# Performance work log

Measured on AMD Instinct MI355X. Metric: run time of the kernel, lower is better.

The kernel has to match this reference:

```python
import jax, jax.numpy as jnp
import numpy as np

EPS_NORM = 1e-12
BN_EPS = 1e-5

def _l2norm(x, axis=-1):
    n = jnp.sqrt(jnp.sum(x * x, axis=axis, keepdims=True))
    return x / jnp.maximum(n, EPS_NORM)

def setup_inputs() -> dict:
    key = jax.random.key(0)
    ks = jax.random.split(key, 16)
    B, C, H, W, K = 32, 256, 64, 64, 5
    supp_feat = jax.random.normal(ks[0], (B, C, H, W), dtype=jnp.float32)
    supp_mask = (jax.random.uniform(ks[1], (B, 1, H, W)) > 0.5).astype(jnp.float32)
    part_queries = 0.02 * jax.random.normal(ks[2], (1, K, C), dtype=jnp.float32)
    temperature = jnp.array([0.1], dtype=jnp.float32)
    margin = jnp.array([0.15], dtype=jnp.float32)
    q_w = jax.random.normal(ks[3], (C, C), dtype=jnp.float32) / np.sqrt(C)  # 1x1 conv, no bias
    bn_w = 1.0 + 0.1 * jax.random.normal(ks[4], (C,), dtype=jnp.float32)
    bn_b = 0.1 * jax.random.normal(ks[5], (C,), dtype=jnp.float32)
    bn_mean = 0.1 * jax.random.normal(ks[6], (C,), dtype=jnp.float32)
    bn_var = 0.5 + jax.random.uniform(ks[7], (C,), dtype=jnp.float32)
    k_w = jax.random.normal(ks[8], (C, C), dtype=jnp.float32) / np.sqrt(C)
    k_b = 0.01 * jax.random.normal(ks[9], (C,), dtype=jnp.float32)
    v_w = jax.random.normal(ks[10], (C, C), dtype=jnp.float32) / np.sqrt(C)
    v_b = 0.01 * jax.random.normal(ks[11], (C,), dtype=jnp.float32)
    out_w = jax.random.normal(ks[12], (C, C), dtype=jnp.float32) / np.sqrt(C)
    out_b = 0.01 * jax.random.normal(ks[13], (C,), dtype=jnp.float32)
    gamma = jnp.array([0.1], dtype=jnp.float32)  # nonzero so the refine branch contributes
    return {"supp_feat": supp_feat, "supp_mask": supp_mask, "part_queries": part_queries,
            "temperature": temperature, "margin": margin, "q_w": q_w, "bn_w": bn_w,
            "bn_b": bn_b, "bn_mean": bn_mean, "bn_var": bn_var, "k_w": k_w, "k_b": k_b,
            "v_w": v_w, "v_b": v_b, "out_w": out_w, "out_b": out_b, "gamma": gamma}

def reference(supp_feat, supp_mask, part_queries, temperature, margin, q_w, bn_w, bn_b,
              bn_mean, bn_var, k_w, k_b, v_w, v_b, out_w, out_b, gamma):
    B, C, H, W = supp_feat.shape
    K = part_queries.shape[1]
    flat_mask = supp_mask.reshape(B, -1)                       # [B, HW]
    flat_feat = jnp.swapaxes(supp_feat.reshape(B, C, -1), 1, 2)  # [B, HW, C]
    queries_norm = _l2norm(part_queries)[0]                    # [K, C]
    feat_norm = _l2norm(flat_feat)                             # [B, HW, C]
    temp = jnp.maximum(temperature, 0.01)[0]
    sim = jnp.einsum('kc,bnc->bkn', queries_norm, feat_norm) / temp  # [B, K, HW]
    sim = jnp.where(flat_mask[:, None, :] > 0, sim, -jnp.inf)
    attn = jnp.nan_to_num(jax.nn.softmax(sim, axis=-1), nan=0.0)
    part_tokens = jnp.einsum('bkn,bnc->bkc', attn, flat_feat)  # [B, K, C]
    # diversity loss
    nt = _l2norm(part_tokens)
    cos = jnp.einsum('bkc,bjc->bkj', nt, nt) * (1.0 - jnp.eye(K, dtype=supp_feat.dtype))
    m = jnp.clip(margin, 0.0, 0.5)[0]
    div_loss = jnp.maximum(cos - m, 0.0).sum() / (B * K * (K - 1) + 1e-5)
    # refine attention
    q = jnp.einsum('oc,bchw->bohw', q_w, supp_feat)            # 1x1 conv, no bias
    scale = bn_w / jnp.sqrt(bn_var + BN_EPS)
    q = q * scale[None, :, None, None] + (bn_b - bn_mean * scale)[None, :, None, None]
    Q = jnp.swapaxes(q.reshape(B, C, -1), 1, 2)                # [B, HW, C]
    Kt = part_tokens @ k_w.T + k_b                             # [B, K, C]
    Vt = part_tokens @ v_w.T + v_b
    refine = jax.nn.softmax(jnp.einsum('bnc,bkc->bnk', Q, Kt) / (C ** 0.5), axis=-1)
    attn_out = jnp.einsum('bnk,bkc->bnc', refine, Vt)          # [B, HW, C]
    attn_out = jnp.swapaxes(attn_out, 1, 2).reshape(B, C, H, W)
    attn_out = jnp.einsum('oc,bchw->bohw', out_w, attn_out) + out_b[None, :, None, None]
    enhanced = supp_feat + gamma[0] * attn_out
    return (enhanced, div_loss, part_tokens)
```

## Files before the change

### kernel.cpp

```cpp
#include <hip/hip_runtime.h>
#include <hip/hip_bf16.h>
#include <math.h>

#define B_  32
#define C_  256
#define HW_ 4096
#define K_  5
#define P_  128
#define NT_ 32
#define PS_ 68

typedef __hip_bfloat16 bf16;
typedef unsigned int u32;
typedef __attribute__((ext_vector_type(8))) short bf16x8;
typedef __attribute__((ext_vector_type(4))) float f32x4;

template<bool BF>
__device__ inline float LD(const void* p, size_t i) {
    if (BF) return __bfloat162float(((const bf16*)p)[i]);
    return ((const float*)p)[i];
}
template<bool BF>
__device__ inline void ST(void* p, size_t i, float v) {
    if (BF) ((bf16*)p)[i] = __float2bfloat16(v);
    else    ((float*)p)[i] = v;
}
template<bool BF>
__device__ inline float4 LD4(const void* p, size_t i) {
    if (BF) {
        ushort4 u = *(const ushort4*)((const unsigned short*)p + i);
        float4 r;
        r.x = __uint_as_float(((u32)u.x) << 16);
        r.y = __uint_as_float(((u32)u.y) << 16);
        r.z = __uint_as_float(((u32)u.z) << 16);
        r.w = __uint_as_float(((u32)u.w) << 16);
        return r;
    }
    return *(const float4*)((const float*)p + i);
}
template<bool BF>
__device__ inline void ST2(void* p, size_t i, float2 v) {
    if (BF) {
        bf16 a = __float2bfloat16(v.x), b = __float2bfloat16(v.y);
        ushort2 u;
        u.x = *(unsigned short*)&a; u.y = *(unsigned short*)&b;
        *(ushort2*)((unsigned short*)p + i) = u;
    } else {
        *(float2*)((float*)p + i) = v;
    }
}
__device__ inline u32 packbf2(float a, float b) {
    bf16 x = __float2bfloat16(a), y = __float2bfloat16(b);
    return (((u32)*(unsigned short*)&y) << 16) | (u32)(*(unsigned short*)&x);
}
__device__ inline float lo16f(u32 u) { return __uint_as_float(u << 16); }
__device__ inline float hi16f(u32 u) { return __uint_as_float(u & 0xffff0000u); }

__device__ int detect_bf(const void* feat, int* cntL) {
    int t = threadIdx.x;
    if (t == 0) *cntL = 0;
    __syncthreads();
    const unsigned short* u = (const unsigned short*)feat;
    int local = 0;
    for (int i = t; i < 4096; i += blockDim.x) {
        float v = __uint_as_float(((u32)u[i]) << 16);
        float a = fabsf(v);
        local += (a >= 1e-4f && a <= 100.f) ? 1 : 0;
    }
    for (int o = 32; o > 0; o >>= 1) local += __shfl_down(local, o, 64);
    if ((t & 63) == 0) atomicAdd(cntL, local);
    __syncthreads();
    return (*cntL > 3072) ? 1 : 0;
}

__device__ inline float blk_sum(float v, float* sh) {
    for (int o = 32; o > 0; o >>= 1) v += __shfl_down(v, o, 64);
    int w = threadIdx.x >> 6;
    __syncthreads();
    if ((threadIdx.x & 63) == 0) sh[w] = v;
    __syncthreads();
    return sh[0] + sh[1] + sh[2] + sh[3];
}

template<bool BF>
__device__ void simpt_body(const void* feat, const void* mask, const void* temp,
                           const void* pq, float* ptp, float* mz, float* smem) {
    u32*   featB = (u32*)smem;
    float* red   = smem + 17408;
    u32*   wB    = (u32*)red;
    float* qL    = smem + 17408 + 1536;
    float* simL  = qL;
    float* sc    = qL + 1280;
    int t = threadIdx.x, lane = t & 63, q = t >> 6;
    int b = blockIdx.y, tile = blockIdx.x;

    if (q < K_) {
        float4 v = LD4<BF>(pq, (size_t)q * C_ + lane * 4);
        float ss = v.x * v.x + v.y * v.y + v.z * v.z + v.w * v.w;
        for (int o = 32; o > 0; o >>= 1) ss += __shfl_xor(ss, o, 64);
        float inv = 1.0f / fmaxf(sqrtf(ss), 1e-12f);
        *(float4*)(qL + q * C_ + lane * 4) =
            make_float4(v.x * inv, v.y * inv, v.z * inv, v.w * inv);
    }
    if (t == 0) sc[0] = 1.0f / fmaxf(LD<BF>(temp, 0), 0.01f);
    __syncthreads();

    int c0 = q * 32, half = lane >> 5, lm = lane & 31;
    float sa[4] = {0.f, 0.f, 0.f, 0.f};
    float da[K_][4];
    #pragma unroll
    for (int k = 0; k < K_; k++)
        #pragma unroll
        for (int i = 0; i < 4; i++) da[k][i] = 0.f;
    size_t gbase = (size_t)b * C_ * HW_ + (size_t)tile * P_ + lm * 4;
    #pragma unroll 4
    for (int j = 0; j < 16; j++) {
        int c = c0 + 2 * j + half;
        float4 f = LD4<BF>(feat, gbase + (size_t)c * HW_);
        sa[0] += f.x * f.x; sa[1] += f.y * f.y; sa[2] += f.z * f.z; sa[3] += f.w * f.w;
        #pragma unroll
        for (int k = 0; k < K_; k++) {
            float qv = qL[k * C_ + c];
            da[k][0] += f.x * qv; da[k][1] += f.y * qv;
            da[k][2] += f.z * qv; da[k][3] += f.w * qv;
        }
        *(uint2*)&featB[c * PS_ + 2 * lm] =
            make_uint2(packbf2(f.x, f.y), packbf2(f.z, f.w));
    }
    #pragma unroll
    for (int i = 0; i < 4; i++) sa[i] += __shfl_down(sa[i], 32, 64);
    #pragma unroll
    for (int k = 0; k < K_; k++)
        #pragma unroll
        for (int i = 0; i < 4; i++) da[k][i] += __shfl_down(da[k][i], 32, 64);

    float tinv = sc[0];
    for (int r = 0; r < 4; r++) {
        if (lane < 32) {
            red[0 * 256 + q * 32 + lane] = sa[r];
            #pragma unroll
            for (int k = 0; k < K_; k++) red[(1 + k) * 256 + q * 32 + lane] = da[k][r];
        }
        __syncthreads();
        if (t < 160) {
            int kk = t >> 5, m = t & 31, n = 4 * m + r;
            float ssum = 0.f, dsum = 0.f;
            #pragma unroll
            for (int g = 0; g < 8; g++) {
                ssum += red[0 * 256 + g * 32 + m];
                dsum += red[(1 + kk) * 256 + g * 32 + m];
            }
            float mval = LD<BF>(mask, (size_t)b * HW_ + tile * P_ + n);
            simL[kk * P_ + n] = (mval > 0.f)
                ? dsum * (tinv / fmaxf(sqrtf(ssum), 1e-12f)) : -INFINITY;
        }
        __syncthreads();
    }

    if (q < K_) {
        float s0 = simL[q * P_ + 2 * lane], s1 = simL[q * P_ + 2 * lane + 1];
        float m = fmaxf(s0, s1);
        for (int o = 32; o > 0; o >>= 1) m = fmaxf(m, __shfl_xor(m, o, 64));
        float e0 = (s0 == -INFINITY) ? 0.f : __expf(s0 - m);
        float e1 = (s1 == -INFINITY) ? 0.f : __expf(s1 - m);
        float z = e0 + e1;
        for (int o = 32; o > 0; o >>= 1) z += __shfl_xor(z, o, 64);
        wB[q * PS_ + lane] = packbf2(e0, e1);
        if (lane == 0) {
            size_t mzb = ((size_t)(b * NT_ + tile) * K_ + q) * 2;
            mz[mzb] = m; mz[mzb + 1] = z;
        }
    }
    __syncthreads();

    int r16 = lane & 15, g = lane >> 4;
    size_t pb = (size_t)(b * NT_ + tile) * (K_ * C_);
    #pragma unroll
    for (int sub = 0; sub < 2; sub++) {
        int ctile = q * 32 + sub * 16;
        f32x4 acc = {0.f, 0.f, 0.f, 0.f};
        #pragma unroll
        for (int s = 0; s < 4; s++) {
            bf16x8 a = *(const bf16x8*)(featB + (ctile + r16) * PS_ + 16 * s + 4 * g);
            bf16x8 bb = *(const bf16x8*)(wB + r16 * PS_ + 16 * s + 4 * g);
            acc = __builtin_amdgcn_mfma_f32_16x16x32_bf16(a, bb, acc, 0, 0, 0);
        }
        if (r16 < K_) {
            #pragma unroll
            for (int r = 0; r < 4; r++)
                ptp[pb + (size_t)r16 * C_ + ctile + 4 * g + r] = acc[r];
        }
    }
}
__global__ __launch_bounds__(512, 4) void k_simpt(const void* feat, const void* mask,
                                                  const void* temp, const void* pq,
                                                  float* ptp, float* mz) {
    __shared__ __attribute__((aligned(16))) float smem[20232];
    __shared__ int cnt;
    int flg = detect_bf(feat, &cnt);
    if (flg) simpt_body<true >(feat, mask, temp, pq, ptp, mz, smem);
    else     simpt_body<false>(feat, mask, temp, pq, ptp, mz, smem);
}

__device__ inline float merge_one(const float* ptp, const float* mz,
                                  int b, int kk, int c) {
    float M = -INFINITY;
    #pragma unroll 8
    for (int tl = 0; tl < NT_; tl++)
        M = fmaxf(M, mz[((size_t)(b * NT_ + tl) * K_ + kk) * 2]);
    float Zs = 0.f, acc = 0.f;
    #pragma unroll 8
    for (int tl = 0; tl < NT_; tl++) {
        size_t mzb = ((size_t)(b * NT_ + tl) * K_ + kk) * 2;
        float m_t = mz[mzb], z_t = mz[mzb + 1];
        float s = (m_t == -INFINITY) ? 0.f : __expf(m_t - M);
        Zs += z_t * s;
        acc += ptp[(size_t)(b * NT_ + tl) * (K_ * C_) + kk * C_ + c] * s;
    }
    return (Zs > 0.f) ? acc / Zs : 0.f;
}
template<bool BF>
__device__ void prep_part(const void* qw, const void* kw, const void* kb,
                          const void* vw, const void* vb, const void* ow,
                          const void* bnw, const void* bnb, const void* bnm,
                          const void* bnv, float ptv, int bk,
                          float* W2, float* b2, float* OV, float* pt, float* smem) {
    float* ptL = smem;
    float* KtL = smem + 256;
    float* VtL = smem + 512;
    float* sh  = smem + 768;
    int t = threadIdx.x;
    ptL[t] = ptv;
    pt[(size_t)bk * C_ + t] = ptv;
    __syncthreads();
    float kt = LD<BF>(kb, t), vt = LD<BF>(vb, t);
    for (int c = 0; c < C_; c += 4) {
        float4 p4 = *(float4*)(ptL + c);
        float4 kw4 = LD4<BF>(kw, (size_t)t * C_ + c);
        float4 vw4 = LD4<BF>(vw, (size_t)t * C_ + c);
        kt += kw4.x * p4.x + kw4.y * p4.y + kw4.z * p4.z + kw4.w * p4.w;
        vt += vw4.x * p4.x + vw4.y * p4.y + vw4.z * p4.z + vw4.w * p4.w;
    }
    float scale = LD<BF>(bnw, t) * rsqrtf(LD<BF>(bnv, t) + 1e-5f);
    float shift = LD<BF>(bnb, t) - LD<BF>(bnm, t) * scale;
    KtL[t] = kt * scale;
    VtL[t] = vt;
    float bpart = kt * shift;
    __syncthreads();
    float ov = 0;
    for (int c = 0; c < C_; c += 4) {
        float4 v4 = *(float4*)(VtL + c);
        float4 ow4 = LD4<BF>(ow, (size_t)t * C_ + c);
        ov += ow4.x * v4.x + ow4.y * v4.y + ow4.z * v4.z + ow4.w * v4.w;
    }
    OV[(size_t)bk * C_ + t] = ov;
    float w2 = 0;
    for (int o = 0; o < C_; o++) w2 += KtL[o] * LD<BF>(qw, (size_t)o * C_ + t);
    W2[(size_t)bk * C_ + t] = w2 * (1.0f / 16.0f);
    float bs = blk_sum(bpart, sh);
    if (t == 0) b2[bk] = bs * (1.0f / 16.0f);
}
template<bool BF>
__device__ void div_part(const float* ptp, const float* mz, const void* margin,
                         float* divpart, float* smem) {
    float* ptL = smem;
    float* rn  = smem + K_ * C_;
    float* sh  = rn + 8;
    int b = blockIdx.x - B_ * K_, t = threadIdx.x;
    for (int kk = 0; kk < K_; kk++) ptL[kk * C_ + t] = merge_one(ptp, mz, b, kk, t);
    __syncthreads();
    for (int k = 0; k < K_; k++) {
        float v = ptL[k * C_ + t];
        float s = blk_sum(v * v, sh);
        if (t == 0) rn[k] = 1.0f / fmaxf(sqrtf(s), 1e-12f);
    }
    __syncthreads();
    float m = LD<BF>(margin, 0);
    m = fminf(fmaxf(m, 0.f), 0.5f);
    int p = t >> 3, g = t & 7;
    float contrib = 0.f;
    if (p < K_ * K_) {
        int k = p / K_, j = p % K_;
        float d = 0;
        for (int c = g; c < C_; c += 8) d += ptL[k * C_ + c] * ptL[j * C_ + c];
        d += __shfl_down(d, 4, 8);
        d += __shfl_down(d, 2, 8);
        d += __shfl_down(d, 1, 8);
        if (g == 0 && k != j) contrib = fmaxf(d * rn[k] * rn[j] - m, 0.f);
    }
    float s = blk_sum(contrib, sh);
    if (t == 0) divpart[b] = s;
}
template<bool BF>
__device__ void mergeprep_body(const void* qw, const void* kw, const void* kb,
                               const void* vw, const void* vb, const void* ow,
                               const void* bnw, const void* bnb, const void* bnm,
                               const void* bnv, const void* margin,
                               const float* ptp, const float* mz,
                               float* W2, float* b2, float* OV, float* pt,
                               float* divpart, float* smem) {
    int bid = blockIdx.x, t = threadIdx.x;
    if (bid < B_ * K_) {
        int b = bid / K_, kk = bid % K_;
        float ptv = merge_one(ptp, mz, b, kk, t);
        prep_part<BF>(qw, kw, kb, vw, vb, ow, bnw, bnb, bnm, bnv,
                      ptv, bid, W2, b2, OV, pt, smem);
    } else {
        div_part<BF>(ptp, mz, margin, divpart, smem);
    }
}
__global__ void k_mergeprep(const void* feat, const void* qw, const void* kw,
                            const void* kb, const void* vw, const void* vb,
                            const void* ow, const void* bnw, const void* bnb,
                            const void* bnm, const void* bnv, const void* margin,
                            const float* ptp, const float* mz,
                            float* W2, float* b2, float* OV, float* pt, float* divpart) {
    __shared__ __attribute__((aligned(16))) float smem[K_ * C_ + 16];
    __shared__ int cnt;
    int flg = detect_bf(feat, &cnt);
    if (flg) mergeprep_body<true >(qw, kw, kb, vw, vb, ow, bnw, bnb, bnm, bnv, margin,
                                   ptp, mz, W2, b2, OV, pt, divpart, smem);
    else     mergeprep_body<false>(qw, kw, kb, vw, vb, ow, bnw, bnb, bnm, bnv, margin,
                                   ptp, mz, W2, b2, OV, pt, divpart, smem);
}

template<bool BF>
__device__ void fin_body(const void* feat, const void* outb, const void* gamma,
                         const float* W2, const float* b2, const float* OV,
                         const float* pt, const float* divpart,
                         void* dout, float* smem) {
    u32*   featU = (u32*)smem;
    float* red   = smem + 16384;
    float* eL    = red + 1280;
    u32*   W2p   = (u32*)(eL + 640);
    u32*   OVp   = W2p + 640;
    float* obL   = (float*)(OVp + 640);
    float* b2L   = obL + 256;
    int t = threadIdx.x, lane = t & 63, q = t >> 6;
    int b = blockIdx.y, tile = blockIdx.x;
    for (int i = t; i < 640; i += 512) {
        W2p[i] = packbf2(W2[(size_t)b * 1280 + 2 * i], W2[(size_t)b * 1280 + 2 * i + 1]);
        OVp[i] = packbf2(OV[(size_t)b * 1280 + 2 * i], OV[(size_t)b * 1280 + 2 * i + 1]);
    }
    if (t < C_) obL[t] = LD<BF>(outb, t);
    if (t < K_) b2L[t] = b2[b * K_ + t];
    __syncthreads();

    int c0 = q * 32, half = lane >> 5, lm = lane & 31;
    size_t gbase = (size_t)b * C_ * HW_ + (size_t)tile * P_ + lm * 4;
    float la[K_][4];
    #pragma unroll
    for (int k = 0; k < K_; k++)
        #pragma unroll
        for (int i = 0; i < 4; i++) la[k][i] = 0.f;
    #pragma unroll 4
    for (int j = 0; j < 16; j++) {
        int c = c0 + 2 * j + half;
        float4 f = LD4<BF>(feat, gbase + (size_t)c * HW_);
        #pragma unroll
        for (int k = 0; k < K_; k++) {
            u32 u = W2p[k * 128 + (c >> 1)];
            float wv = half ? hi16f(u) : lo16f(u);
            la[k][0] += f.x * wv; la[k][1] += f.y * wv;
            la[k][2] += f.z * wv; la[k][3] += f.w * wv;
        }
        int ps = lm ^ (c & 31);
        *(uint2*)&featU[c * 64 + 2 * ps] =
            make_uint2(packbf2(f.x, f.y), packbf2(f.z, f.w));
    }
    #pragma unroll
    for (int k = 0; k < K_; k++)
        #pragma unroll
        for (int i = 0; i < 4; i++) la[k][i] += __shfl_down(la[k][i], 32, 64);

    for (int r = 0; r < 4; r++) {
        if (lane < 32) {
            #pragma unroll
            for (int k = 0; k < K_; k++) red[k * 256 + q * 32 + lane] = la[k][r];
        }
        __syncthreads();
        if (t < 32) {
            int n = 4 * t + r;
            float lg[K_];
            #pragma unroll
            for (int k = 0; k < K_; k++) {
                float s = b2L[k];
                #pragma unroll
                for (int g = 0; g < 8; g++) s += red[k * 256 + g * 32 + t];
                lg[k] = s;
            }
            float mx = fmaxf(fmaxf(fmaxf(lg[0], lg[1]), fmaxf(lg[2], lg[3])), lg[4]);
            float e0 = __expf(lg[0] - mx), e1 = __expf(lg[1] - mx),
                  e2 = __expf(lg[2] - mx), e3 = __expf(lg[3] - mx),
                  e4 = __expf(lg[4] - mx);
            float inv = 1.0f / (e0 + e1 + e2 + e3 + e4);
            eL[0 * P_ + n] = e0 * inv; eL[1 * P_ + n] = e1 * inv;
            eL[2 * P_ + n] = e2 * inv; eL[3 * P_ + n] = e3 * inv;
            eL[4 * P_ + n] = e4 * inv;
        }
        __syncthreads();
    }

    float g = LD<BF>(gamma, 0);
    float2 ek[K_];
    #pragma unroll
    for (int k = 0; k < K_; k++) ek[k] = *(const float2*)(eL + k * P_ + 2 * lane);
    size_t obase = (size_t)b * C_ * HW_ + (size_t)tile * P_ + 2 * lane;
    #pragma unroll 4
    for (int cc = 0; cc < 32; cc++) {
        int c = c0 + cc, x = c & 31;
        u32 v = featU[c * 64 + 2 * ((lane >> 1) ^ x) + (lane & 1)];
        float f0 = lo16f(v), f1 = hi16f(v);
        float ob = obL[c];
        float a0 = ob, a1 = ob;
        #pragma unroll
        for (int k = 0; k < K_; k++) {
            u32 u = OVp[k * 128 + (c >> 1)];
            float ov = (c & 1) ? hi16f(u) : lo16f(u);
            a0 += ek[k].x * ov; a1 += ek[k].y * ov;
        }
        ST2<BF>(dout, obase + (size_t)c * HW_, make_float2(f0 + g * a0, f1 + g * a1));
    }
    if (b == 0) {
        const size_t enh = (size_t)B_ * C_ * HW_;
        for (int i = blockIdx.x * 512 + t; i < B_ * K_ * C_; i += NT_ * 512)
            ST<BF>(dout, enh + 1 + i, pt[i]);
        if (blockIdx.x == 0 && t == 0) {
            float s = 0;
            for (int bb = 0; bb < B_; bb++) s += divpart[bb];
            ST<BF>(dout, enh, s / (640.0f + 1e-5f));
        }
    }
}
__global__ __launch_bounds__(512, 4) void k_fin(const void* feat, const void* outb,
                                                const void* gamma, const float* W2,
                                                const float* b2, const float* OV,
                                                const float* pt, const float* divpart,
                                                void* dout) {
    __shared__ __attribute__((aligned(16))) float smem[19848];
    __shared__ int cnt;
    int flg = detect_bf(feat, &cnt);
    if (flg) fin_body<true >(feat, outb, gamma, W2, b2, OV, pt, divpart, dout, smem);
    else     fin_body<false>(feat, outb, gamma, W2, b2, OV, pt, divpart, dout, smem);
}

extern "C" void kernel_launch(void* const* d_in, const int* in_sizes, int n_in,
                              void* d_out, int out_size, void* d_ws, size_t ws_size,
                              hipStream_t stream) {
    const void* feat = d_in[0];
    const void* mask = d_in[1];
    const void* pq   = d_in[2];
    const void* temp = d_in[3];
    const void* marg = d_in[4];
    const void* qw   = d_in[5];
    const void* bnw  = d_in[6];
    const void* bnb  = d_in[7];
    const void* bnm  = d_in[8];
    const void* bnv  = d_in[9];
    const void* kw   = d_in[10];
    const void* kb   = d_in[11];
    const void* vw   = d_in[12];
    const void* vb   = d_in[13];
    const void* ow   = d_in[14];
    const void* ob   = d_in[15];
    const void* gm   = d_in[16];

    float* ws  = (float*)d_ws;
    float* ptp = ws;
    float* mz  = ptp + (size_t)B_ * NT_ * K_ * C_;
    float* pt  = mz  + (size_t)B_ * NT_ * K_ * 2;
    float* W2  = pt  + B_ * K_ * C_;
    float* b2  = W2  + B_ * K_ * C_;
    float* OV  = b2  + B_ * K_;
    float* dvp = OV  + B_ * K_ * C_;

    hipLaunchKernelGGL(k_simpt, dim3(NT_, B_), dim3(512), 0, stream,
                       feat, mask, temp, pq, ptp, mz);
    hipLaunchKernelGGL(k_mergeprep, dim3(B_ * K_ + B_), dim3(256), 0, stream,
                       feat, qw, kw, kb, vw, vb, ow, bnw, bnb, bnm, bnv, marg,
                       ptp, mz, W2, b2, OV, pt, dvp);
    hipLaunchKernelGGL(k_fin, dim3(NT_, B_), dim3(512), 0, stream,
                       feat, ob, gm, W2, b2, OV, pt, dvp, d_out);
}
```

Before: 148.5 us.

## Compute refine output projection with MFMA and fold gamma and bias into operands

```diff
diff --git a/kernel.cpp b/kernel.cpp
--- a/kernel.cpp
+++ b/kernel.cpp
@@ -9,6 +9,7 @@
 #define P_  128
 #define NT_ 32
 #define PS_ 68
+#define FS_ 66
 
 typedef __hip_bfloat16 bf16;
 typedef unsigned int u32;
@@ -37,17 +38,6 @@
         return r;
     }
     return *(const float4*)((const float*)p + i);
-}
-template<bool BF>
-__device__ inline void ST2(void* p, size_t i, float2 v) {
-    if (BF) {
-        bf16 a = __float2bfloat16(v.x), b = __float2bfloat16(v.y);
-        ushort2 u;
-        u.x = *(unsigned short*)&a; u.y = *(unsigned short*)&b;
-        *(ushort2*)((unsigned short*)p + i) = u;
-    } else {
-        *(float2*)((float*)p + i) = v;
-    }
 }
 __device__ inline u32 packbf2(float a, float b) {
     bf16 x = __float2bfloat16(a), y = __float2bfloat16(b);
@@ -330,19 +320,33 @@
                          const float* pt, const float* divpart,
                          void* dout, float* smem) {
     u32*   featU = (u32*)smem;
-    float* red   = smem + 16384;
-    float* eL    = red + 1280;
-    u32*   W2p   = (u32*)(eL + 640);
-    u32*   OVp   = W2p + 640;
-    float* obL   = (float*)(OVp + 640);
-    float* b2L   = obL + 256;
+    u32*   OVp8  = featU + 256 * FS_;
+    u32*   eT8   = OVp8 + 1024;
+    u32*   zb    = eT8 + 512;
+    float* pool  = (float*)(zb + 4);
+    u32*   W2p   = (u32*)pool;
+    float* red   = pool;
+    float* b2L   = pool + 1280;
     int t = threadIdx.x, lane = t & 63, q = t >> 6;
     int b = blockIdx.y, tile = blockIdx.x;
+
+    float g0 = LD<BF>(gamma, 0);
     for (int i = t; i < 640; i += 512) {
         W2p[i] = packbf2(W2[(size_t)b * 1280 + 2 * i], W2[(size_t)b * 1280 + 2 * i + 1]);
-        OVp[i] = packbf2(OV[(size_t)b * 1280 + 2 * i], OV[(size_t)b * 1280 + 2 * i + 1]);
-    }
-    if (t < C_) obL[t] = LD<BF>(outb, t);
+    }
+    if (t < 256) {
+        float o0 = OV[(size_t)b * 1280 + 0 * C_ + t] * g0;
+        float o1 = OV[(size_t)b * 1280 + 1 * C_ + t] * g0;
+        float o2 = OV[(size_t)b * 1280 + 2 * C_ + t] * g0;
+        float o3 = OV[(size_t)b * 1280 + 3 * C_ + t] * g0;
+        float o4 = OV[(size_t)b * 1280 + 4 * C_ + t] * g0;
+        float obv = LD<BF>(outb, t) * g0;
+        OVp8[t * 4 + 0] = packbf2(o0, o1);
+        OVp8[t * 4 + 1] = packbf2(o2, o3);
+        OVp8[t * 4 + 2] = packbf2(o4, obv);
+        OVp8[t * 4 + 3] = 0u;
+    }
+    if (t < 4) zb[t] = 0u;
     if (t < K_) b2L[t] = b2[b * K_ + t];
     __syncthreads();
 
@@ -364,14 +368,14 @@
             la[k][0] += f.x * wv; la[k][1] += f.y * wv;
             la[k][2] += f.z * wv; la[k][3] += f.w * wv;
         }
-        int ps = lm ^ (c & 31);
-        *(uint2*)&featU[c * 64 + 2 * ps] =
+        *(uint2*)&featU[c * FS_ + 2 * lm] =
             make_uint2(packbf2(f.x, f.y), packbf2(f.z, f.w));
     }
     #pragma unroll
     for (int k = 0; k < K_; k++)
         #pragma unroll
         for (int i = 0; i < 4; i++) la[k][i] += __shfl_down(la[k][i], 32, 64);
+    __syncthreads();
 
     for (int r = 0; r < 4; r++) {
         if (lane < 32) {
@@ -386,7 +390,7 @@
             for (int k = 0; k < K_; k++) {
                 float s = b2L[k];
                 #pragma unroll
-                for (int g = 0; g < 8; g++) s += red[k * 256 + g * 32 + t];
+                for (int gg = 0; gg < 8; gg++) s += red[k * 256 + gg * 32 + t];
                 lg[k] = s;
             }
             float mx = fmaxf(fmaxf(fmaxf(lg[0], lg[1]), fmaxf(lg[2], lg[3])), lg[4]);
@@ -394,32 +398,36 @@
                   e2 = __expf(lg[2] - mx), e3 = __expf(lg[3] - mx),
                   e4 = __expf(lg[4] - mx);
             float inv = 1.0f / (e0 + e1 + e2 + e3 + e4);
-            eL[0 * P_ + n] = e0 * inv; eL[1 * P_ + n] = e1 * inv;
-            eL[2 * P_ + n] = e2 * inv; eL[3 * P_ + n] = e3 * inv;
-            eL[4 * P_ + n] = e4 * inv;
+            eT8[n * 4 + 0] = packbf2(e0 * inv, e1 * inv);
+            eT8[n * 4 + 1] = packbf2(e2 * inv, e3 * inv);
+            eT8[n * 4 + 2] = packbf2(e4 * inv, 1.0f);
+            eT8[n * 4 + 3] = 0u;
         }
         __syncthreads();
     }
 
-    float g = LD<BF>(gamma, 0);
-    float2 ek[K_];
-    #pragma unroll
-    for (int k = 0; k < K_; k++) ek[k] = *(const float2*)(eL + k * P_ + 2 * lane);
-    size_t obase = (size_t)b * C_ * HW_ + (size_t)tile * P_ + 2 * lane;
-    #pragma unroll 4
-    for (int cc = 0; cc < 32; cc++) {
-        int c = c0 + cc, x = c & 31;
-        u32 v = featU[c * 64 + 2 * ((lane >> 1) ^ x) + (lane & 1)];
-        float f0 = lo16f(v), f1 = hi16f(v);
-        float ob = obL[c];
-        float a0 = ob, a1 = ob;
-        #pragma unroll
-        for (int k = 0; k < K_; k++) {
-            u32 u = OVp[k * 128 + (c >> 1)];
-            float ov = (c & 1) ? hi16f(u) : lo16f(u);
-            a0 += ek[k].x * ov; a1 += ek[k].y * ov;
-        }
-        ST2<BF>(dout, obase + (size_t)c * HW_, make_float2(f0 + g * a0, f1 + g * a1));
+    int r16 = lane & 15, gg = lane >> 4;
+    const bf16x8 zfrag = *(const bf16x8*)zb;
+    size_t base = (size_t)b * C_ * HW_ + (size_t)tile * P_;
+    #pragma unroll
+    for (int ct = 0; ct < 2; ct++) {
+        int ctile = (q * 2 + ct) * 16;
+        bf16x8 a = (gg == 0) ? *(const bf16x8*)(OVp8 + (ctile + r16) * 4) : zfrag;
+        #pragma unroll
+        for (int pt8 = 0; pt8 < 8; pt8++) {
+            int ptile = pt8 * 16;
+            bf16x8 bb = (gg == 0) ? *(const bf16x8*)(eT8 + (ptile + r16) * 4) : zfrag;
+            f32x4 acc = {0.f, 0.f, 0.f, 0.f};
+            acc = __builtin_amdgcn_mfma_f32_16x16x32_bf16(a, bb, acc, 0, 0, 0);
+            int p = ptile + r16;
+            #pragma unroll
+            for (int r = 0; r < 4; r++) {
+                int c = ctile + 4 * gg + r;
+                u32 w = featU[c * FS_ + (p >> 1)];
+                float f = (p & 1) ? hi16f(w) : lo16f(w);
+                ST<BF>(dout, base + (size_t)c * HW_ + p, f + acc[r]);
+            }
+        }
     }
     if (b == 0) {
         const size_t enh = (size_t)B_ * C_ * HW_;
@@ -427,7 +435,7 @@
             ST<BF>(dout, enh + 1 + i, pt[i]);
         if (blockIdx.x == 0 && t == 0) {
             float s = 0;
-            for (int bb = 0; bb < B_; bb++) s += divpart[bb];
+            for (int bb2 = 0; bb2 < B_; bb2++) s += divpart[bb2];
             ST<BF>(dout, enh, s / (640.0f + 1e-5f));
         }
     }
@@ -437,7 +445,7 @@
                                                 const float* b2, const float* OV,
                                                 const float* pt, const float* divpart,
                                                 void* dout) {
-    __shared__ __attribute__((aligned(16))) float smem[19848];
+    __shared__ __attribute__((aligned(16))) float smem[19728];
     __shared__ int cnt;
     int flg = detect_bf(feat, &cnt);
     if (flg) fin_body<true >(feat, outb, gamma, W2, b2, OV, pt, divpart, dout, smem);
```

Result: faster. 142.5 us (-4.0%).
